# Performance work log

Hardware: AMD Instinct MI355X
Metric: run time of the kernel (lower is better)

## Reference

```python
import jax, jax.numpy as jnp
from jax import lax
import numpy as np

B, N, D = 8, 8192, 64
NPOINT, RADIUS, NSAMPLE = 1024, 0.2, 32
EPS = 1e-5  # BatchNorm eps


def setup_inputs() -> dict:
    key = jax.random.key(0)
    ks = jax.random.split(key, 8)
    inp = {
        "xyz": jax.random.uniform(ks[0], (B, 3, N), dtype=jnp.float32),
        "points": jax.random.normal(ks[1], (B, D, N), dtype=jnp.float32),
    }
    dims = [(3 + D, 64), (64, 64), (64, 128)]
    for i, (ci, co) in enumerate(dims):
        inp[f"w{i}"] = jax.random.normal(ks[2 + i], (co, ci), dtype=jnp.float32) * float(1.0 / np.sqrt(ci))
        inp[f"b{i}"] = jnp.zeros((co,), jnp.float32)
        inp[f"g{i}"] = jnp.ones((co,), jnp.float32)
        inp[f"beta{i}"] = jnp.zeros((co,), jnp.float32)
    return inp


def _fps(xyz):
    # Farthest point sampling. xyz: [B, N, 3] -> idx [B, NPOINT]
    b = xyz.shape[0]

    def step(carry, _):
        dist, farthest = carry  # dist [B,N], farthest [B]
        centroid = jnp.take_along_axis(xyz, farthest[:, None, None], axis=1)  # [B,1,3]
        d = jnp.sum((xyz - centroid) ** 2, axis=-1)  # [B,N]
        dist = jnp.minimum(dist, d)
        return (dist, jnp.argmax(dist, axis=-1).astype(jnp.int32)), farthest

    init = (jnp.full((b, xyz.shape[1]), 1e10, xyz.dtype), jnp.zeros((b,), jnp.int32))
    _, idxs = lax.scan(step, init, None, length=NPOINT)  # [NPOINT, B]
    return idxs.T  # [B, NPOINT]


def _ball_query(new_xyz, xyz):
    # new_xyz: [B,S,3] centers, xyz: [B,N,3] -> neighbor idx [B,S,NSAMPLE]
    n = xyz.shape[1]
    sqr = jnp.sum((new_xyz[:, :, None, :] - xyz[:, None, :, :]) ** 2, axis=-1)  # [B,S,N]
    cand = jnp.where(sqr > RADIUS * RADIUS, n, jnp.arange(n, dtype=jnp.int32))  # N = invalid
    neg_top, _ = lax.top_k(-cand, NSAMPLE)  # smallest NSAMPLE valid indices
    idx = -neg_top  # [B,S,K], ascending; == n where fewer than K neighbors
    first = idx[..., :1]  # pad with first (closest-by-index) valid neighbor
    return jnp.where(idx == n, first, idx)


def reference(xyz, points, w0, b0, g0, beta0, w1, b1, g1, beta1, w2, b2, g2, beta2):
    xyz_t = jnp.transpose(xyz, (0, 2, 1))      # [B,N,3]
    pts_t = jnp.transpose(points, (0, 2, 1))   # [B,N,D]
    fps_idx = _fps(xyz_t)                      # [B,S]
    bidx = jnp.arange(xyz.shape[0])[:, None]
    new_xyz = xyz_t[bidx, fps_idx]             # [B,S,3]
    idx = _ball_query(new_xyz, xyz_t)          # [B,S,K]
    bidx3 = jnp.arange(xyz.shape[0])[:, None, None]
    grouped_xyz = xyz_t[bidx3, idx]            # [B,S,K,3]
    grouped_norm = grouped_xyz - new_xyz[:, :, None, :]
    grouped_pts = pts_t[bidx3, idx]            # [B,S,K,D]
    feat = jnp.concatenate([grouped_norm, grouped_pts], axis=-1)  # [B,S,K,3+D]
    # shared 1x1 Conv + BatchNorm (training-mode batch stats) + ReLU chain
    for w, b, g, bt in ((w0, b0, g0, beta0), (w1, b1, g1, beta1), (w2, b2, g2, beta2)):
        h = jnp.einsum('bskc,oc->bsko', feat, w) + b
        mean = jnp.mean(h, axis=(0, 1, 2), keepdims=True)
        var = jnp.var(h, axis=(0, 1, 2), keepdims=True)
        feat = jax.nn.relu((h - mean) * lax.rsqrt(var + EPS) * g + bt)
    pooled = jnp.max(feat, axis=2)             # max over NSAMPLE -> [B,S,C_out]
    return jnp.transpose(new_xyz, (0, 2, 1)), jnp.transpose(pooled, (0, 2, 1))
```

## Files before the change

kernel.cpp:

```cpp
#include <hip/hip_runtime.h>

#define NB 8
#define NP 8192
#define SP 1024
#define KS 32
#define CD 64
#define MROWS (NB*SP*KS)
#define NCOPY 16

typedef float v2f __attribute__((ext_vector_type(2)));
typedef unsigned long long u64;

template <int CTRL>
__device__ __forceinline__ u64 dpp_max_step(u64 x) {
    int lo = (int)(unsigned)(x & 0xffffffffull);
    int hi = (int)(unsigned)(x >> 32);
    int slo = __builtin_amdgcn_update_dpp(lo, lo, CTRL, 0xf, 0xf, false);
    int shi = __builtin_amdgcn_update_dpp(hi, hi, CTRL, 0xf, 0xf, false);
    u64 y = ((u64)(unsigned)shi << 32) | (unsigned)slo;
    return x > y ? x : y;
}

__global__ __launch_bounds__(512, 1) void k_fps_pre(const float* __restrict__ xyz,
                                                    float* __restrict__ fps_pts,
                                                    float* __restrict__ out_nx,
                                                    const float* __restrict__ points,
                                                    float* __restrict__ pts_t,
                                                    const float* __restrict__ w0,
                                                    const float* __restrict__ w1,
                                                    const float* __restrict__ w2,
                                                    float* __restrict__ Wt0,
                                                    float* __restrict__ Wt1,
                                                    float* __restrict__ Wt2,
                                                    float* __restrict__ stats)
{
#pragma clang fp contract(off)
    __shared__ __align__(16) unsigned char smem[131072 + 256];
    const int blk = blockIdx.x;
    const int t = threadIdx.x;

    if (blk >= NB) {
        if (blk >= NB + NB * (NP / 64)) {
            for (int i = t; i < 8192; i += 512) stats[i] = 0.f;
            for (int i = t; i < 64 * 67; i += 512) { int c = i / 67, kk = i % 67; Wt0[kk * 64 + c] = w0[i]; }
            for (int i = t; i < 64 * 64; i += 512) { int c = i >> 6, kk = i & 63; Wt1[kk * 64 + c] = w1[i]; }
            for (int i = t; i < 128 * 64; i += 512) { int c = i >> 6, kk = i & 63; Wt2[kk * 128 + c] = w2[i]; }
            return;
        }
        float (*tile)[65] = (float(*)[65])smem;
        const int tblk = blk - NB;
        const int b = tblk >> 7;
        const int n0 = (tblk & 127) << 6;
        const float* pb = points + (size_t)b * CD * NP;
        const int c = t & 63;
        const int dr = t >> 6;
#pragma unroll
        for (int it = 0; it < 8; ++it) {
            int d = dr + it * 8;
            tile[d][c] = pb[(size_t)d * NP + n0 + c];
        }
        __syncthreads();
#pragma unroll
        for (int it = 0; it < 8; ++it) {
            int nn = dr + it * 8;
            pts_t[((size_t)b * NP + n0 + nn) * CD + c] = tile[c][nn];
        }
        return;
    }

    float4* s_p = (float4*)smem;
    u64 (*s_wk)[8] = (u64(*)[8])(smem + 131072);
    const int b = blk;
    const int lane = t & 63, wid = t >> 6;
    const float* xb = xyz + (size_t)b * 3 * NP;
    v2f px[8], py[8], pz[8], dv[8];
#pragma unroll
    for (int j = 0; j < 8; ++j) {
        const int n0 = t + (2 * j) * 512, n1 = n0 + 512;
        px[j] = (v2f){xb[n0], xb[n1]};
        py[j] = (v2f){xb[NP + n0], xb[NP + n1]};
        pz[j] = (v2f){xb[2 * NP + n0], xb[2 * NP + n1]};
        dv[j] = (v2f){1e10f, 1e10f};
        s_p[n0] = make_float4(px[j].x, py[j].x, pz[j].x, 0.f);
        s_p[n1] = make_float4(px[j].y, py[j].y, pz[j].y, 0.f);
    }
    float cx = xb[0], cy = xb[NP], cz = xb[2 * NP];
    float hx0 = 0.f, hy0 = 0.f, hz0 = 0.f;
    float hx1 = 0.f, hy1 = 0.f, hz1 = 0.f;
    __syncthreads();
    for (int i = 0; i < SP; ++i) {
        if (i == t)       { hx0 = cx; hy0 = cy; hz0 = cz; }
        if (i == t + 512) { hx1 = cx; hy1 = cy; hz1 = cz; }
        float bv = -1.f; int bg = 0;
#pragma unroll
        for (int j = 0; j < 8; ++j) {
            v2f dx = px[j] - cx;
            v2f dy = py[j] - cy;
            v2f dz = pz[j] - cz;
            v2f d  = dx * dx + dy * dy;
            d = d + dz * dz;
            v2f dm = dv[j];
            dm.x = fminf(dm.x, d.x);
            dm.y = fminf(dm.y, d.y);
            dv[j] = dm;
            if (dm.x > bv) { bv = dm.x; bg = t + (2 * j) * 512; }
            if (dm.y > bv) { bv = dm.y; bg = t + (2 * j + 1) * 512; }
        }
        u64 bk = ((u64)__float_as_uint(bv) << 32) | (unsigned int)~bg;
        bk = dpp_max_step<0x111>(bk);
        bk = dpp_max_step<0x112>(bk);
        bk = dpp_max_step<0x114>(bk);
        bk = dpp_max_step<0x118>(bk);
        bk = dpp_max_step<0x142>(bk);
        bk = dpp_max_step<0x143>(bk);
        const int par = i & 1;
        if (lane == 63) s_wk[par][wid] = bk;
        __syncthreads();
        u64 rk = s_wk[par][lane & 7];
        rk = dpp_max_step<0x111>(rk);
        rk = dpp_max_step<0x112>(rk);
        rk = dpp_max_step<0x114>(rk);
        rk = dpp_max_step<0x118>(rk);
        const int wg = ~__builtin_amdgcn_readlane((int)(unsigned)(rk & 0xffffffffull), 15);
        const float4 c = s_p[wg];
        cx = c.x; cy = c.y; cz = c.z;
    }
    fps_pts[(b * SP + t) * 3 + 0] = hx0;
    fps_pts[(b * SP + t) * 3 + 1] = hy0;
    fps_pts[(b * SP + t) * 3 + 2] = hz0;
    fps_pts[(b * SP + t + 512) * 3 + 0] = hx1;
    fps_pts[(b * SP + t + 512) * 3 + 1] = hy1;
    fps_pts[(b * SP + t + 512) * 3 + 2] = hz1;
    out_nx[(size_t)b * 3 * SP + 0 * SP + t] = hx0;
    out_nx[(size_t)b * 3 * SP + 1 * SP + t] = hy0;
    out_nx[(size_t)b * 3 * SP + 2 * SP + t] = hz0;
    out_nx[(size_t)b * 3 * SP + 0 * SP + t + 512] = hx1;
    out_nx[(size_t)b * 3 * SP + 1 * SP + t + 512] = hy1;
    out_nx[(size_t)b * 3 * SP + 2 * SP + t + 512] = hz1;
}

__global__ __launch_bounds__(256) void k_ballquery(const float* __restrict__ xyz,
                                                   const float* __restrict__ fps_pts,
                                                   int* __restrict__ ball_idx)
{
    const int wib = threadIdx.x >> 6;
    const int lane = threadIdx.x & 63;
    const int wid = blockIdx.x * 4 + wib;
    const int b = wid >> 10;
    const float* xb = xyz + (size_t)b * 3 * NP;
    const float qx = fps_pts[wid * 3 + 0];
    const float qy = fps_pts[wid * 3 + 1];
    const float qz = fps_pts[wid * 3 + 2];
    __shared__ int s_list[4][KS];
    int* list = s_list[wib];
    const float r2 = (float)(0.2 * 0.2);
    int found = 0;
    for (int base = 0; base < NP && found < KS; base += 64) {
        int n = base + lane;
        float dx = __fsub_rn(qx, xb[n]);
        float dy = __fsub_rn(qy, xb[NP + n]);
        float dz = __fsub_rn(qz, xb[2 * NP + n]);
        float d = __fadd_rn(__fadd_rn(__fmul_rn(dx, dx), __fmul_rn(dy, dy)), __fmul_rn(dz, dz));
        bool in = !(d > r2);
        unsigned long long m = __ballot(in);
        int before = __popcll(m & ((1ull << lane) - 1ull));
        int pos = found + before;
        if (in && pos < KS) list[pos] = n;
        found += __popcll(m);
    }
    int first = list[0];
    if (lane < KS) {
        int v = (lane < found) ? list[lane] : first;
        ball_idx[wid * KS + lane] = v;
    }
}

__global__ __launch_bounds__(256) void k_layer1(const float* __restrict__ xyz,
                                                const float* __restrict__ pts_t,
                                                const float* __restrict__ fps_pts,
                                                const int* __restrict__ ball_idx,
                                                const float* __restrict__ Wt0,
                                                const float* __restrict__ bias0,
                                                float* __restrict__ h1,
                                                float* __restrict__ sum0,
                                                float* __restrict__ ssq0)
{
    __shared__ __align__(16) float Ft[67 * 128];
    __shared__ __align__(16) float Ws[67 * 64];
    __shared__ int   s_idx[128];
    __shared__ float s_q[4][3];
    const int t = threadIdx.x;
    const int m0 = blockIdx.x * 128;
    const int g0 = m0 >> 5;
    const int b = g0 >> 10;
    if (t < 128) s_idx[t] = ball_idx[g0 * KS + t];
    if (t < 12) ((float*)s_q)[t] = fps_pts[g0 * 3 + t];
    for (int i = t; i < 67 * 64; i += 256) Ws[i] = Wt0[i];
    __syncthreads();
    {
        const int r = t >> 1, half = t & 1;
        const int n = s_idx[r];
        const float* prow = pts_t + ((size_t)b * NP + n) * CD;
#pragma unroll
        for (int rep = 0; rep < 8; ++rep) {
            const int c4 = half * 4 + rep * 8;
            float4 v = *(const float4*)(prow + c4);
            Ft[(3 + c4 + 0) * 128 + r] = v.x;
            Ft[(3 + c4 + 1) * 128 + r] = v.y;
            Ft[(3 + c4 + 2) * 128 + r] = v.z;
            Ft[(3 + c4 + 3) * 128 + r] = v.w;
        }
        if (t < 128) {
            const int n2 = s_idx[t];
            const int g = t >> 5;
            const float* xb = xyz + (size_t)b * 3 * NP;
            Ft[0 * 128 + t] = __fsub_rn(xb[n2],          s_q[g][0]);
            Ft[1 * 128 + t] = __fsub_rn(xb[NP + n2],     s_q[g][1]);
            Ft[2 * 128 + t] = __fsub_rn(xb[2 * NP + n2], s_q[g][2]);
        }
    }
    __syncthreads();
    const int rg = t >> 3;
    const int cg = t & 7;
    float4 ba = *(const float4*)(bias0 + cg * 8);
    float4 bb = *(const float4*)(bias0 + cg * 8 + 4);
    float acc[4][8];
#pragma unroll
    for (int j = 0; j < 4; ++j) {
        acc[j][0] = ba.x; acc[j][1] = ba.y; acc[j][2] = ba.z; acc[j][3] = ba.w;
        acc[j][4] = bb.x; acc[j][5] = bb.y; acc[j][6] = bb.z; acc[j][7] = bb.w;
    }
    for (int kk = 0; kk < 67; ++kk) {
        float4 f = *(const float4*)(Ft + kk * 128 + rg * 4);
        float4 wa = *(const float4*)(Ws + kk * 64 + cg * 8);
        float4 wb = *(const float4*)(Ws + kk * 64 + cg * 8 + 4);
        float fv[4] = {f.x, f.y, f.z, f.w};
        float wv[8] = {wa.x, wa.y, wa.z, wa.w, wb.x, wb.y, wb.z, wb.w};
#pragma unroll
        for (int j = 0; j < 4; ++j)
#pragma unroll
            for (int i = 0; i < 8; ++i) acc[j][i] = fmaf(fv[j], wv[i], acc[j][i]);
    }
    float ls[8] = {0,0,0,0,0,0,0,0}, lq[8] = {0,0,0,0,0,0,0,0};
#pragma unroll
    for (int j = 0; j < 4; ++j) {
        int m = m0 + rg * 4 + j;
        float4 oa = {acc[j][0], acc[j][1], acc[j][2], acc[j][3]};
        float4 ob = {acc[j][4], acc[j][5], acc[j][6], acc[j][7]};
        *(float4*)(h1 + (size_t)m * 64 + cg * 8) = oa;
        *(float4*)(h1 + (size_t)m * 64 + cg * 8 + 4) = ob;
#pragma unroll
        for (int i = 0; i < 8; ++i) { float v = acc[j][i]; ls[i] += v; lq[i] += v * v; }
    }
    __syncthreads();
    float* part_s = Ft;
    float* part_q = Ft + 2048;
#pragma unroll
    for (int i = 0; i < 8; ++i) { part_s[rg * 64 + cg * 8 + i] = ls[i]; part_q[rg * 64 + cg * 8 + i] = lq[i]; }
    __syncthreads();
    if (t < 64) {
        float s = 0.f, q = 0.f;
#pragma unroll
        for (int rgi = 0; rgi < 32; ++rgi) { s += part_s[rgi * 64 + t]; q += part_q[rgi * 64 + t]; }
        int cp = blockIdx.x & (NCOPY - 1);
        atomicAdd(&sum0[cp * 64 + t], s);
        atomicAdd(&ssq0[cp * 64 + t], q);
    }
}

__global__ __launch_bounds__(256) void k_layer2(const float* __restrict__ h1,
                                                const float* __restrict__ Wt1,
                                                const float* __restrict__ bias1,
                                                const float* __restrict__ ss1,
                                                float* __restrict__ h2,
                                                float* __restrict__ sum1,
                                                float* __restrict__ ssq1)
{
    __shared__ __align__(16) float Ft[64 * 128];
    __shared__ __align__(16) float Ws[64 * 64];
    __shared__ float s_sc[64], s_sh[64];
    const int t = threadIdx.x;
    const int m0 = blockIdx.x * 128;
    for (int i = t; i < 64 * 64; i += 256) Ws[i] = Wt1[i];
    if (t < 64) { s_sc[t] = ss1[t]; s_sh[t] = ss1[64 + t]; }
    __syncthreads();
    {
        const int tq = t >> 2, qq = t & 3;
#pragma unroll
        for (int rr = 0; rr < 2; ++rr) {
            const int r = rr * 64 + tq;
            const float* hrow = h1 + (size_t)(m0 + r) * 64;
#pragma unroll
            for (int rep = 0; rep < 4; ++rep) {
                const int c4 = qq * 4 + rep * 16;
                float4 v = *(const float4*)(hrow + c4);
                Ft[(c4 + 0) * 128 + r] = fmaxf(0.f, fmaf(v.x, s_sc[c4 + 0], s_sh[c4 + 0]));
                Ft[(c4 + 1) * 128 + r] = fmaxf(0.f, fmaf(v.y, s_sc[c4 + 1], s_sh[c4 + 1]));
                Ft[(c4 + 2) * 128 + r] = fmaxf(0.f, fmaf(v.z, s_sc[c4 + 2], s_sh[c4 + 2]));
                Ft[(c4 + 3) * 128 + r] = fmaxf(0.f, fmaf(v.w, s_sc[c4 + 3], s_sh[c4 + 3]));
// ... 184 lines not shown
    float rstd = 1.0f / sqrtf(var + 1e-5f);
    float scale = g[c] * rstd;
    ss[c] = scale;
    ss[nc + c] = beta[c] - mean * scale;
}

extern "C" void kernel_launch(void* const* d_in, const int* in_sizes, int n_in,
                              void* d_out, int out_size, void* d_ws, size_t ws_size,
                              hipStream_t stream)
{
    const float* xyz    = (const float*)d_in[0];
    const float* points = (const float*)d_in[1];
    const float* w0 = (const float*)d_in[2];
    const float* b0 = (const float*)d_in[3];
    const float* gm0 = (const float*)d_in[4];
    const float* bt0 = (const float*)d_in[5];
    const float* w1 = (const float*)d_in[6];
    const float* b1 = (const float*)d_in[7];
    const float* gm1 = (const float*)d_in[8];
    const float* bt1 = (const float*)d_in[9];
    const float* w2 = (const float*)d_in[10];
    const float* b2 = (const float*)d_in[11];
    const float* gm2 = (const float*)d_in[12];
    const float* bt2 = (const float*)d_in[13];
    float* out = (float*)d_out;

    char* p = (char*)d_ws;
    auto alloc = [&](size_t nbytes) -> void* {
        void* r = (void*)p;
        p += (nbytes + 255) & ~(size_t)255;
        return r;
    };
    float* fps_pts = (float*)alloc((size_t)NB * SP * 3 * 4);
    int*   ball_idx = (int*)alloc((size_t)NB * SP * KS * 4);
    float* pts_t = (float*)alloc((size_t)NB * NP * CD * 4);
    float* h1 = (float*)alloc((size_t)MROWS * 64 * 4);
    float* h2 = (float*)alloc((size_t)MROWS * 64 * 4);
    float* gmax = (float*)alloc((size_t)NB * SP * 128 * 4);
    float* gmin = (float*)alloc((size_t)NB * SP * 128 * 4);
    float* Wt0 = (float*)alloc(67 * 64 * 4);
    float* Wt1 = (float*)alloc(64 * 64 * 4);
    float* Wt2 = (float*)alloc(64 * 128 * 4);
    float* stats = (float*)alloc(8192 * 4);
    float* ss1 = (float*)alloc(128 * 4);
    float* ss2 = (float*)alloc(128 * 4);
    float* ss3 = (float*)alloc(256 * 4);

    float* sum0 = stats;
    float* ssq0 = stats + 16 * 64;
    float* sum1 = stats + 2 * 16 * 64;
    float* ssq1 = stats + 3 * 16 * 64;
    float* sum2 = stats + 4 * 16 * 64;
    float* ssq2 = sum2 + 16 * 128;

    k_fps_pre<<<NB + NB * (NP / 64) + 1, 512, 0, stream>>>(
        xyz, fps_pts, out, points, pts_t, w0, w1, w2, Wt0, Wt1, Wt2, stats);
    k_ballquery<<<(NB * SP) / 4, 256, 0, stream>>>(xyz, fps_pts, ball_idx);
    k_layer1<<<MROWS / 128, 256, 0, stream>>>(xyz, pts_t, fps_pts, ball_idx, Wt0, b0, h1, sum0, ssq0);
    k_finalize<<<1, 128, 0, stream>>>(sum0, ssq0, gm0, bt0, ss1, 64);
    k_layer2<<<MROWS / 128, 256, 0, stream>>>(h1, Wt1, b1, ss1, h2, sum1, ssq1);
    k_finalize<<<1, 128, 0, stream>>>(sum1, ssq1, gm1, bt1, ss2, 64);
    k_layer3<<<MROWS / 128, 256, 0, stream>>>(h2, Wt2, b2, ss2, sum2, ssq2, gmax, gmin);
    k_finalize<<<1, 128, 0, stream>>>(sum2, ssq2, gm2, bt2, ss3, 128);
    k_pool2<<<(NB * SP * 128) / 256, 256, 0, stream>>>(gmax, gmin, ss3, out + 24576);
}
```

Before: 1.217 ms.

## Split FPS argmax into float max then index min, use packed-math distance asm

The FPS loop now reduces a plain float max across the wavefront with DPP, then finds the matching slot and reduces the smallest global index in a separate 32-bit DPP pass. This replaces the 64-bit key shuffles and the per-element index tracking. Distances are computed with inline packed-f32 asm using negated centroids. The cross-wave reduction is shortened by one step, and selected centroids are written out by thread 0 on each iteration instead of being buffered per thread. The intent is to shorten the serial per-iteration critical path of FPS, at the cost of extra compare and select work and per-iteration global stores.

```diff
diff --git a/kernel.cpp b/kernel.cpp
--- a/kernel.cpp
+++ b/kernel.cpp
@@ -19,6 +19,19 @@
     int shi = __builtin_amdgcn_update_dpp(hi, hi, CTRL, 0xf, 0xf, false);
     u64 y = ((u64)(unsigned)shi << 32) | (unsigned)slo;
     return x > y ? x : y;
+}
+
+template <int CTRL>
+__device__ __forceinline__ float dpp_fmax_step(float x) {
+    int xi = __float_as_int(x);
+    int s = __builtin_amdgcn_update_dpp(xi, xi, CTRL, 0xf, 0xf, false);
+    return fmaxf(x, __int_as_float(s));
+}
+
+template <int CTRL>
+__device__ __forceinline__ int dpp_imin_step(int x) {
+    int s = __builtin_amdgcn_update_dpp(x, x, CTRL, 0xf, 0xf, false);
+    return s < x ? s : x;
 }
 
 __global__ __launch_bounds__(512, 1) void k_fps_pre(const float* __restrict__ xyz,
@@ -73,6 +86,8 @@
     const int b = blk;
     const int lane = t & 63, wid = t >> 6;
     const float* xb = xyz + (size_t)b * 3 * NP;
+    float* fp_b = fps_pts + (size_t)b * SP * 3;
+    float* nx_b = out_nx + (size_t)b * 3 * SP;
     v2f px[8], py[8], pz[8], dv[8];
 #pragma unroll
     for (int j = 0; j < 8; ++j) {
@@ -84,59 +99,81 @@
         s_p[n0] = make_float4(px[j].x, py[j].x, pz[j].x, 0.f);
         s_p[n1] = make_float4(px[j].y, py[j].y, pz[j].y, 0.f);
     }
-    float cx = xb[0], cy = xb[NP], cz = xb[2 * NP];
-    float hx0 = 0.f, hy0 = 0.f, hz0 = 0.f;
-    float hx1 = 0.f, hy1 = 0.f, hz1 = 0.f;
+    {
+        const float cx = xb[0], cy = xb[NP], cz = xb[2 * NP];
+        if (t == 0) {
+            fp_b[0] = cx; fp_b[1] = cy; fp_b[2] = cz;
+            nx_b[0] = cx; nx_b[SP] = cy; nx_b[2 * SP] = cz;
+        }
+    }
+    v2f ncx = (v2f){-xb[0], -xb[0]};
+    v2f ncy = (v2f){-xb[NP], -xb[NP]};
+    v2f ncz = (v2f){-xb[2 * NP], -xb[2 * NP]};
     __syncthreads();
     for (int i = 0; i < SP; ++i) {
-        if (i == t)       { hx0 = cx; hy0 = cy; hz0 = cz; }
-        if (i == t + 512) { hx1 = cx; hy1 = cy; hz1 = cz; }
-        float bv = -1.f; int bg = 0;
+        float bv = -1.f;
 #pragma unroll
         for (int j = 0; j < 8; ++j) {
-            v2f dx = px[j] - cx;
-            v2f dy = py[j] - cy;
-            v2f dz = pz[j] - cz;
-            v2f d  = dx * dx + dy * dy;
-            d = d + dz * dz;
+            v2f t0, t1, d;
+            asm("v_pk_add_f32 %0, %3, %6\n\t"
+                "v_pk_add_f32 %1, %4, %7\n\t"
+                "v_pk_add_f32 %2, %5, %8\n\t"
+                "v_pk_mul_f32 %0, %0, %0\n\t"
+                "v_pk_mul_f32 %1, %1, %1\n\t"
+                "v_pk_add_f32 %0, %0, %1\n\t"
+                "v_pk_mul_f32 %2, %2, %2\n\t"
+                "v_pk_add_f32 %2, %2, %0"
+                : "=&v"(t0), "=&v"(t1), "=&v"(d)
+                : "v"(px[j]), "v"(py[j]), "v"(pz[j]), "v"(ncx), "v"(ncy), "v"(ncz));
             v2f dm = dv[j];
             dm.x = fminf(dm.x, d.x);
             dm.y = fminf(dm.y, d.y);
             dv[j] = dm;
-            if (dm.x > bv) { bv = dm.x; bg = t + (2 * j) * 512; }
-            if (dm.y > bv) { bv = dm.y; bg = t + (2 * j + 1) * 512; }
-        }
-        u64 bk = ((u64)__float_as_uint(bv) << 32) | (unsigned int)~bg;
-        bk = dpp_max_step<0x111>(bk);
-        bk = dpp_max_step<0x112>(bk);
-        bk = dpp_max_step<0x114>(bk);
-        bk = dpp_max_step<0x118>(bk);
-        bk = dpp_max_step<0x142>(bk);
-        bk = dpp_max_step<0x143>(bk);
+            bv = fmaxf(bv, fmaxf(dm.x, dm.y));
+        }
+        float wv = bv;
+        wv = dpp_fmax_step<0x111>(wv);
+        wv = dpp_fmax_step<0x112>(wv);
+        wv = dpp_fmax_step<0x114>(wv);
+        wv = dpp_fmax_step<0x118>(wv);
+        wv = dpp_fmax_step<0x142>(wv);
+        wv = dpp_fmax_step<0x143>(wv);
+        const float Wv = __int_as_float(__builtin_amdgcn_readlane(__float_as_int(wv), 63));
+        int slot = 16;
+#pragma unroll
+        for (int j = 7; j >= 0; --j) {
+            if (dv[j].y == Wv) slot = 2 * j + 1;
+            if (dv[j].x == Wv) slot = 2 * j;
+        }
+        int gid = (slot << 9) | t;
+        gid = dpp_imin_step<0x111>(gid);
+        gid = dpp_imin_step<0x112>(gid);
+        gid = dpp_imin_step<0x114>(gid);
+        gid = dpp_imin_step<0x118>(gid);
+        gid = dpp_imin_step<0x142>(gid);
+        gid = dpp_imin_step<0x143>(gid);
         const int par = i & 1;
-        if (lane == 63) s_wk[par][wid] = bk;
+        if (lane == 63)
+            s_wk[par][wid] = ((u64)(unsigned)__float_as_int(wv) << 32) | (unsigned)~gid;
         __syncthreads();
         u64 rk = s_wk[par][lane & 7];
         rk = dpp_max_step<0x111>(rk);
         rk = dpp_max_step<0x112>(rk);
         rk = dpp_max_step<0x114>(rk);
-        rk = dpp_max_step<0x118>(rk);
-        const int wg = ~__builtin_amdgcn_readlane((int)(unsigned)(rk & 0xffffffffull), 15);
+        const int wg = ~__builtin_amdgcn_readlane((int)(unsigned)(rk & 0xffffffffull), 7);
         const float4 c = s_p[wg];
-        cx = c.x; cy = c.y; cz = c.z;
-    }
-    fps_pts[(b * SP + t) * 3 + 0] = hx0;
-    fps_pts[(b * SP + t) * 3 + 1] = hy0;
-    fps_pts[(b * SP + t) * 3 + 2] = hz0;
-    fps_pts[(b * SP + t + 512) * 3 + 0] = hx1;
-    fps_pts[(b * SP + t + 512) * 3 + 1] = hy1;
-    fps_pts[(b * SP + t + 512) * 3 + 2] = hz1;
-    out_nx[(size_t)b * 3 * SP + 0 * SP + t] = hx0;
-    out_nx[(size_t)b * 3 * SP + 1 * SP + t] = hy0;
-    out_nx[(size_t)b * 3 * SP + 2 * SP + t] = hz0;
-    out_nx[(size_t)b * 3 * SP + 0 * SP + t + 512] = hx1;
-    out_nx[(size_t)b * 3 * SP + 1 * SP + t + 512] = hy1;
-    out_nx[(size_t)b * 3 * SP + 2 * SP + t + 512] = hz1;
+        if (t == 0 && i + 1 < SP) {
+            fp_b[(i + 1) * 3 + 0] = c.x;
+            fp_b[(i + 1) * 3 + 1] = c.y;
+            fp_b[(i + 1) * 3 + 2] = c.z;
+            nx_b[i + 1] = c.x;
+            nx_b[SP + i + 1] = c.y;
+            nx_b[2 * SP + i + 1] = c.z;
+        }
+        ncx = (v2f){-c.x, -c.x};
+        ncy = (v2f){-c.y, -c.y};
+        ncz = (v2f){-c.z, -c.z};
+    }
 }
 
 __global__ __launch_bounds__(256) void k_ballquery(const float* __restrict__ xyz,
```

New measurement: 1.327 ms. +9.0%, slower.

## Fuse FPS, ball query and layer1 into persistent producer-consumer megakernel

Applied to the files above, without the earlier changes.

Merges farthest point sampling, ball query and the first conv layer into one persistent kernel. Eight blocks run FPS and publish sampled centroids in chunks of 32 through global atomics and a progress counter. The remaining blocks take work items from an atomic ticket, spin until their centroids are ready, then run the ball query and layer1 GEMM, so this work overlaps with the serial FPS. In exchange it adds spin-waiting, atomic traffic and reduced occupancy (512-thread blocks, half idle in the GEMM). It also depends on all 256 blocks being co-resident, or it can deadlock.

```diff
diff --git a/kernel.cpp b/kernel.cpp
--- a/kernel.cpp
+++ b/kernel.cpp
@@ -21,250 +21,280 @@
     return x > y ? x : y;
 }
 
-__global__ __launch_bounds__(512, 1) void k_fps_pre(const float* __restrict__ xyz,
-                                                    float* __restrict__ fps_pts,
-                                                    float* __restrict__ out_nx,
-                                                    const float* __restrict__ points,
-                                                    float* __restrict__ pts_t,
-                                                    const float* __restrict__ w0,
-                                                    const float* __restrict__ w1,
-                                                    const float* __restrict__ w2,
-                                                    float* __restrict__ Wt0,
-                                                    float* __restrict__ Wt1,
-                                                    float* __restrict__ Wt2,
-                                                    float* __restrict__ stats)
-{
-#pragma clang fp contract(off)
-    __shared__ __align__(16) unsigned char smem[131072 + 256];
+__global__ __launch_bounds__(512) void k_pre(const float* __restrict__ points,
+                                             float* __restrict__ pts_t,
+                                             const float* __restrict__ w0,
+                                             const float* __restrict__ w1,
+                                             const float* __restrict__ w2,
+                                             float* __restrict__ Wt0,
+                                             float* __restrict__ Wt1,
+                                             float* __restrict__ Wt2,
+                                             float* __restrict__ stats,
+                                             int* __restrict__ ctl)
+{
+    __shared__ float tile[64][65];
     const int blk = blockIdx.x;
     const int t = threadIdx.x;
-
-    if (blk >= NB) {
-        if (blk >= NB + NB * (NP / 64)) {
-            for (int i = t; i < 8192; i += 512) stats[i] = 0.f;
-            for (int i = t; i < 64 * 67; i += 512) { int c = i / 67, kk = i % 67; Wt0[kk * 64 + c] = w0[i]; }
-            for (int i = t; i < 64 * 64; i += 512) { int c = i >> 6, kk = i & 63; Wt1[kk * 64 + c] = w1[i]; }
-            for (int i = t; i < 128 * 64; i += 512) { int c = i >> 6, kk = i & 63; Wt2[kk * 128 + c] = w2[i]; }
-            return;
-        }
-        float (*tile)[65] = (float(*)[65])smem;
-        const int tblk = blk - NB;
-        const int b = tblk >> 7;
-        const int n0 = (tblk & 127) << 6;
-        const float* pb = points + (size_t)b * CD * NP;
-        const int c = t & 63;
-        const int dr = t >> 6;
-#pragma unroll
-        for (int it = 0; it < 8; ++it) {
-            int d = dr + it * 8;
-            tile[d][c] = pb[(size_t)d * NP + n0 + c];
-        }
-        __syncthreads();
-#pragma unroll
-        for (int it = 0; it < 8; ++it) {
-            int nn = dr + it * 8;
-            pts_t[((size_t)b * NP + n0 + nn) * CD + c] = tile[c][nn];
-        }
+    if (blk >= NB * (NP / 64)) {
+        for (int i = t; i < 8192; i += 512) stats[i] = 0.f;
+        if (t < 64) ctl[t] = 0;
+        for (int i = t; i < 64 * 67; i += 512) { int c = i / 67, kk = i % 67; Wt0[kk * 64 + c] = w0[i]; }
+        for (int i = t; i < 64 * 64; i += 512) { int c = i >> 6, kk = i & 63; Wt1[kk * 64 + c] = w1[i]; }
+        for (int i = t; i < 128 * 64; i += 512) { int c = i >> 6, kk = i & 63; Wt2[kk * 128 + c] = w2[i]; }
         return;
     }
-
-    float4* s_p = (float4*)smem;
-    u64 (*s_wk)[8] = (u64(*)[8])(smem + 131072);
-    const int b = blk;
+    const int b = blk >> 7;
+    const int n0 = (blk & 127) << 6;
+    const float* pb = points + (size_t)b * CD * NP;
+    const int c = t & 63;
+    const int dr = t >> 6;
+#pragma unroll
+    for (int it = 0; it < 8; ++it) {
+        int d = dr + it * 8;
+        tile[d][c] = pb[(size_t)d * NP + n0 + c];
+    }
+    __syncthreads();
+#pragma unroll
+    for (int it = 0; it < 8; ++it) {
+        int nn = dr + it * 8;
+        pts_t[((size_t)b * NP + n0 + nn) * CD + c] = tile[c][nn];
+    }
+}
+
+__global__ __launch_bounds__(512, 1) void k_mega(const float* __restrict__ xyz,
+                                                 float* __restrict__ fps_pts,
+                                                 float* __restrict__ out_nx,
+                                                 const float* __restrict__ pts_t,
+                                                 const float* __restrict__ Wt0,
+                                                 const float* __restrict__ bias0,
+                                                 float* __restrict__ h1,
+                                                 float* __restrict__ sum0,
+                                                 float* __restrict__ ssq0,
+                                                 int* __restrict__ ctl)
+{
+#pragma clang fp contract(off)
+    __shared__ __align__(16) unsigned char smem[131344];
+    const int blk = blockIdx.x;
+    const int t = threadIdx.x;
     const int lane = t & 63, wid = t >> 6;
-    const float* xb = xyz + (size_t)b * 3 * NP;
-    v2f px[8], py[8], pz[8], dv[8];
-#pragma unroll
-    for (int j = 0; j < 8; ++j) {
-        const int n0 = t + (2 * j) * 512, n1 = n0 + 512;
-        px[j] = (v2f){xb[n0], xb[n1]};
-        py[j] = (v2f){xb[NP + n0], xb[NP + n1]};
-        pz[j] = (v2f){xb[2 * NP + n0], xb[2 * NP + n1]};
-        dv[j] = (v2f){1e10f, 1e10f};
-        s_p[n0] = make_float4(px[j].x, py[j].x, pz[j].x, 0.f);
-        s_p[n1] = make_float4(px[j].y, py[j].y, pz[j].y, 0.f);
-    }
-    float cx = xb[0], cy = xb[NP], cz = xb[2 * NP];
-    float hx0 = 0.f, hy0 = 0.f, hz0 = 0.f;
-    float hx1 = 0.f, hy1 = 0.f, hz1 = 0.f;
-    __syncthreads();
-    for (int i = 0; i < SP; ++i) {
-        if (i == t)       { hx0 = cx; hy0 = cy; hz0 = cz; }
-        if (i == t + 512) { hx1 = cx; hy1 = cy; hz1 = cz; }
-        float bv = -1.f; int bg = 0;
+    unsigned int* fpu = (unsigned int*)fps_pts;
+
+    if (blk < NB) {
+        float4* s_p = (float4*)smem;
+        u64 (*s_wk)[8] = (u64(*)[8])(smem + 131072);
+        const int b = blk;
+        const float* xb = xyz + (size_t)b * 3 * NP;
+        v2f px[8], py[8], pz[8], dv[8];
 #pragma unroll
         for (int j = 0; j < 8; ++j) {
-            v2f dx = px[j] - cx;
-            v2f dy = py[j] - cy;
-            v2f dz = pz[j] - cz;
-            v2f d  = dx * dx + dy * dy;
-            d = d + dz * dz;
-            v2f dm = dv[j];
-            dm.x = fminf(dm.x, d.x);
-            dm.y = fminf(dm.y, d.y);
-            dv[j] = dm;
-            if (dm.x > bv) { bv = dm.x; bg = t + (2 * j) * 512; }
-            if (dm.y > bv) { bv = dm.y; bg = t + (2 * j + 1) * 512; }
-        }
-        u64 bk = ((u64)__float_as_uint(bv) << 32) | (unsigned int)~bg;
-        bk = dpp_max_step<0x111>(bk);
-        bk = dpp_max_step<0x112>(bk);
-        bk = dpp_max_step<0x114>(bk);
-        bk = dpp_max_step<0x118>(bk);
-        bk = dpp_max_step<0x142>(bk);
-        bk = dpp_max_step<0x143>(bk);
-        const int par = i & 1;
-        if (lane == 63) s_wk[par][wid] = bk;
-        __syncthreads();
-        u64 rk = s_wk[par][lane & 7];
-        rk = dpp_max_step<0x111>(rk);
-        rk = dpp_max_step<0x112>(rk);
-        rk = dpp_max_step<0x114>(rk);
-        rk = dpp_max_step<0x118>(rk);
-        const int wg = ~__builtin_amdgcn_readlane((int)(unsigned)(rk & 0xffffffffull), 15);
-        const float4 c = s_p[wg];
-        cx = c.x; cy = c.y; cz = c.z;
-    }
-    fps_pts[(b * SP + t) * 3 + 0] = hx0;
-    fps_pts[(b * SP + t) * 3 + 1] = hy0;
-    fps_pts[(b * SP + t) * 3 + 2] = hz0;
-    fps_pts[(b * SP + t + 512) * 3 + 0] = hx1;
-    fps_pts[(b * SP + t + 512) * 3 + 1] = hy1;
-    fps_pts[(b * SP + t + 512) * 3 + 2] = hz1;
-    out_nx[(size_t)b * 3 * SP + 0 * SP + t] = hx0;
-    out_nx[(size_t)b * 3 * SP + 1 * SP + t] = hy0;
-    out_nx[(size_t)b * 3 * SP + 2 * SP + t] = hz0;
-    out_nx[(size_t)b * 3 * SP + 0 * SP + t + 512] = hx1;
-    out_nx[(size_t)b * 3 * SP + 1 * SP + t + 512] = hy1;
-    out_nx[(size_t)b * 3 * SP + 2 * SP + t + 512] = hz1;
-}
-
-__global__ __launch_bounds__(256) void k_ballquery(const float* __restrict__ xyz,
-                                                   const float* __restrict__ fps_pts,
-                                                   int* __restrict__ ball_idx)
-{
-    const int wib = threadIdx.x >> 6;
-    const int lane = threadIdx.x & 63;
-    const int wid = blockIdx.x * 4 + wib;
-    const int b = wid >> 10;
-    const float* xb = xyz + (size_t)b * 3 * NP;
-    const float qx = fps_pts[wid * 3 + 0];
-    const float qy = fps_pts[wid * 3 + 1];
-    const float qz = fps_pts[wid * 3 + 2];
-    __shared__ int s_list[4][KS];
-    int* list = s_list[wib];
-    const float r2 = (float)(0.2 * 0.2);
-    int found = 0;
-    for (int base = 0; base < NP && found < KS; base += 64) {
-        int n = base + lane;
-        float dx = __fsub_rn(qx, xb[n]);
-        float dy = __fsub_rn(qy, xb[NP + n]);
-        float dz = __fsub_rn(qz, xb[2 * NP + n]);
-        float d = __fadd_rn(__fadd_rn(__fmul_rn(dx, dx), __fmul_rn(dy, dy)), __fmul_rn(dz, dz));
-        bool in = !(d > r2);
-        unsigned long long m = __ballot(in);
-        int before = __popcll(m & ((1ull << lane) - 1ull));
-        int pos = found + before;
-        if (in && pos < KS) list[pos] = n;
-        found += __popcll(m);
-    }
-    int first = list[0];
-    if (lane < KS) {
-        int v = (lane < found) ? list[lane] : first;
-        ball_idx[wid * KS + lane] = v;
-    }
-}
-
-__global__ __launch_bounds__(256) void k_layer1(const float* __restrict__ xyz,
-                                                const float* __restrict__ pts_t,
-                                                const float* __restrict__ fps_pts,
-                                                const int* __restrict__ ball_idx,
-                                                const float* __restrict__ Wt0,
-                                                const float* __restrict__ bias0,
-                                                float* __restrict__ h1,
-                                                float* __restrict__ sum0,
-                                                float* __restrict__ ssq0)
-{
-    __shared__ __align__(16) float Ft[67 * 128];
-    __shared__ __align__(16) float Ws[67 * 64];
-    __shared__ int   s_idx[128];
-    __shared__ float s_q[4][3];
-    const int t = threadIdx.x;
-    const int m0 = blockIdx.x * 128;
-    const int g0 = m0 >> 5;
-    const int b = g0 >> 10;
-    if (t < 128) s_idx[t] = ball_idx[g0 * KS + t];
-    if (t < 12) ((float*)s_q)[t] = fps_pts[g0 * 3 + t];
-    for (int i = t; i < 67 * 64; i += 256) Ws[i] = Wt0[i];
-    __syncthreads();
-    {
-        const int r = t >> 1, half = t & 1;
-        const int n = s_idx[r];
-        const float* prow = pts_t + ((size_t)b * NP + n) * CD;
-#pragma unroll
-        for (int rep = 0; rep < 8; ++rep) {
-            const int c4 = half * 4 + rep * 8;
-            float4 v = *(const float4*)(prow + c4);
-            Ft[(3 + c4 + 0) * 128 + r] = v.x;
-            Ft[(3 + c4 + 1) * 128 + r] = v.y;
-            Ft[(3 + c4 + 2) * 128 + r] = v.z;
-            Ft[(3 + c4 + 3) * 128 + r] = v.w;
-        }
-        if (t < 128) {
-            const int n2 = s_idx[t];
-            const int g = t >> 5;
-            const float* xb = xyz + (size_t)b * 3 * NP;
-            Ft[0 * 128 + t] = __fsub_rn(xb[n2],          s_q[g][0]);
-            Ft[1 * 128 + t] = __fsub_rn(xb[NP + n2],     s_q[g][1]);
-            Ft[2 * 128 + t] = __fsub_rn(xb[2 * NP + n2], s_q[g][2]);
-        }
-    }
-    __syncthreads();
-    const int rg = t >> 3;
-    const int cg = t & 7;
-    float4 ba = *(const float4*)(bias0 + cg * 8);
-    float4 bb = *(const float4*)(bias0 + cg * 8 + 4);
-    float acc[4][8];
-#pragma unroll
-    for (int j = 0; j < 4; ++j) {
-        acc[j][0] = ba.x; acc[j][1] = ba.y; acc[j][2] = ba.z; acc[j][3] = ba.w;
-        acc[j][4] = bb.x; acc[j][5] = bb.y; acc[j][6] = bb.z; acc[j][7] = bb.w;
-    }
-    for (int kk = 0; kk < 67; ++kk) {
-        float4 f = *(const float4*)(Ft + kk * 128 + rg * 4);
-        float4 wa = *(const float4*)(Ws + kk * 64 + cg * 8);
-        float4 wb = *(const float4*)(Ws + kk * 64 + cg * 8 + 4);
-        float fv[4] = {f.x, f.y, f.z, f.w};
-        float wv[8] = {wa.x, wa.y, wa.z, wa.w, wb.x, wb.y, wb.z, wb.w};
-#pragma unroll
-        for (int j = 0; j < 4; ++j)
-#pragma unroll
-            for (int i = 0; i < 8; ++i) acc[j][i] = fmaf(fv[j], wv[i], acc[j][i]);
-    }
-    float ls[8] = {0,0,0,0,0,0,0,0}, lq[8] = {0,0,0,0,0,0,0,0};
-#pragma unroll
-    for (int j = 0; j < 4; ++j) {
-        int m = m0 + rg * 4 + j;
-        float4 oa = {acc[j][0], acc[j][1], acc[j][2], acc[j][3]};
-        float4 ob = {acc[j][4], acc[j][5], acc[j][6], acc[j][7]};
-        *(float4*)(h1 + (size_t)m * 64 + cg * 8) = oa;
-        *(float4*)(h1 + (size_t)m * 64 + cg * 8 + 4) = ob;
-#pragma unroll
-        for (int i = 0; i < 8; ++i) { float v = acc[j][i]; ls[i] += v; lq[i] += v * v; }
-    }
-    __syncthreads();
-    float* part_s = Ft;
-    float* part_q = Ft + 2048;
-#pragma unroll
-    for (int i = 0; i < 8; ++i) { part_s[rg * 64 + cg * 8 + i] = ls[i]; part_q[rg * 64 + cg * 8 + i] = lq[i]; }
-    __syncthreads();
-    if (t < 64) {
-        float s = 0.f, q = 0.f;
-#pragma unroll
-        for (int rgi = 0; rgi < 32; ++rgi) { s += part_s[rgi * 64 + t]; q += part_q[rgi * 64 + t]; }
-        int cp = blockIdx.x & (NCOPY - 1);
-        atomicAdd(&sum0[cp * 64 + t], s);
-        atomicAdd(&ssq0[cp * 64 + t], q);
+            const int n0 = t + (2 * j) * 512, n1 = n0 + 512;
+            px[j] = (v2f){xb[n0], xb[n1]};
+            py[j] = (v2f){xb[NP + n0], xb[NP + n1]};
+            pz[j] = (v2f){xb[2 * NP + n0], xb[2 * NP + n1]};
+            dv[j] = (v2f){1e10f, 1e10f};
+            s_p[n0] = make_float4(px[j].x, py[j].x, pz[j].x, 0.f);
+            s_p[n1] = make_float4(px[j].y, py[j].y, pz[j].y, 0.f);
+        }
+        float cx = xb[0], cy = xb[NP], cz = xb[2 * NP];
+        float hx0 = 0.f, hy0 = 0.f, hz0 = 0.f;
+        float hx1 = 0.f, hy1 = 0.f, hz1 = 0.f;
+        __syncthreads();
+        for (int i = 0; i < SP; ++i) {
+            if (i == t)       { hx0 = cx; hy0 = cy; hz0 = cz; }
+            if (i == t + 512) { hx1 = cx; hy1 = cy; hz1 = cz; }
+            if ((i & 31) == 31) {
+                if (i < 512) {
+                    if (t >= i - 31 && t <= i) {
+                        unsigned int* dst = fpu + ((size_t)b * SP + t) * 3;
+                        atomicExch(dst + 0, __float_as_uint(hx0));
+                        atomicExch(dst + 1, __float_as_uint(hy0));
+                        atomicExch(dst + 2, __float_as_uint(hz0));
+                    }
+                } else {
+                    const int s = t + 512;
+                    if (s >= i - 31 && s <= i) {
+                        unsigned int* dst = fpu + ((size_t)b * SP + s) * 3;
+                        atomicExch(dst + 0, __float_as_uint(hx1));
+                        atomicExch(dst + 1, __float_as_uint(hy1));
+                        atomicExch(dst + 2, __float_as_uint(hz1));
+                    }
+                }
+            }
+            if ((i & 31) == 0 && i != 0 && t == 2) atomicExch(&ctl[8 + b], i);
+            float bv = -1.f; int bg = 0;
+#pragma unroll
+            for (int j = 0; j < 8; ++j) {
+                v2f dx = px[j] - cx;
+                v2f dy = py[j] - cy;
+                v2f dz = pz[j] - cz;
+                v2f d  = dx * dx + dy * dy;
+                d = d + dz * dz;
+                v2f dm = dv[j];
+                dm.x = fminf(dm.x, d.x);
+                dm.y = fminf(dm.y, d.y);
+                dv[j] = dm;
+                if (dm.x > bv) { bv = dm.x; bg = t + (2 * j) * 512; }
+                if (dm.y > bv) { bv = dm.y; bg = t + (2 * j + 1) * 512; }
+            }
+            u64 bk = ((u64)__float_as_uint(bv) << 32) | (unsigned int)~bg;
+            bk = dpp_max_step<0x111>(bk);
+            bk = dpp_max_step<0x112>(bk);
+            bk = dpp_max_step<0x114>(bk);
+            bk = dpp_max_step<0x118>(bk);
+            bk = dpp_max_step<0x142>(bk);
+            bk = dpp_max_step<0x143>(bk);
+            const int par = i & 1;
+            if (lane == 63) s_wk[par][wid] = bk;
+            __syncthreads();
+            u64 rk = s_wk[par][lane & 7];
+            rk = dpp_max_step<0x111>(rk);
+            rk = dpp_max_step<0x112>(rk);
+            rk = dpp_max_step<0x114>(rk);
+            rk = dpp_max_step<0x118>(rk);
+            const int wg = ~__builtin_amdgcn_readlane((int)(unsigned)(rk & 0xffffffffull), 15);
+            const float4 c = s_p[wg];
+            cx = c.x; cy = c.y; cz = c.z;
+        }
+        if (t == 2) atomicExch(&ctl[8 + b], SP);
+        out_nx[(size_t)b * 3 * SP + 0 * SP + t] = hx0;
+        out_nx[(size_t)b * 3 * SP + 1 * SP + t] = hy0;
+        out_nx[(size_t)b * 3 * SP + 2 * SP + t] = hz0;
+        out_nx[(size_t)b * 3 * SP + 0 * SP + t + 512] = hx1;
+        out_nx[(size_t)b * 3 * SP + 1 * SP + t + 512] = hy1;
+        out_nx[(size_t)b * 3 * SP + 2 * SP + t + 512] = hz1;
+        return;
+    }
+
+    float* Ft    = (float*)smem;
+    float* Ws    = (float*)(smem + 34304);
+    int*   s_idx = (int*)(smem + 51456);
+    float* s_q   = (float*)(smem + 51968);
+    int*   s_tk  = (int*)(smem + 131328);
+    int*   s_rdy = (int*)(smem + 131332);
+
+    for (int i = t; i < 67 * 64; i += 512) Ws[i] = Wt0[i];
+
+    for (;;) {
+        __syncthreads();
+        if (t == 0) *s_tk = atomicAdd(&ctl[1], 1);
+        __syncthreads();
+        const int u = *s_tk;
+        if (u >= 2048) break;
+        const int b = u & 7, kq = u >> 3;
+        const int need = 4 * kq + 4;
+        const int g0 = b * SP + kq * 4;
+        for (;;) {
+            if (t == 0) *s_rdy = (atomicAdd(&ctl[8 + b], 0) >= need);
+            __syncthreads();
+            const int ok = *s_rdy;
+            __syncthreads();
+            if (ok) break;
+            __builtin_amdgcn_s_sleep(32);
+        }
+        if (t < 12) {
+            unsigned int uv = atomicAdd(fpu + (size_t)g0 * 3 + t, 0u);
+            s_q[t] = __uint_as_float(uv);
+        }
+        __syncthreads();
+        if (wid < 4) {
+            const float qx = s_q[wid * 3 + 0];
+            const float qy = s_q[wid * 3 + 1];
+            const float qz = s_q[wid * 3 + 2];
+            const float* xbq = xyz + (size_t)b * 3 * NP;
+            int* list = s_idx + wid * KS;
+            const float r2 = (float)(0.2 * 0.2);
+            int found = 0;
+            for (int base2 = 0; base2 < NP && found < KS; base2 += 64) {
+                int n = base2 + lane;
+                float dx = __fsub_rn(qx, xbq[n]);
+                float dy = __fsub_rn(qy, xbq[NP + n]);
+                float dz = __fsub_rn(qz, xbq[2 * NP + n]);
+                float d = __fadd_rn(__fadd_rn(__fmul_rn(dx, dx), __fmul_rn(dy, dy)), __fmul_rn(dz, dz));
+                bool in = !(d > r2);
+                unsigned long long m = __ballot(in);
+                int before = __popcll(m & ((1ull << lane) - 1ull));
+                int pos = found + before;
+                if (in && pos < KS) list[pos] = n;
+                found += __popcll(m);
+            }
+            int first = list[0];
+            if (lane < KS) { int v = (lane < found) ? list[lane] : first; list[lane] = v; }
+        }
+        __syncthreads();
+        const size_t m0 = (size_t)g0 * KS;
+        if (t < 256) {
+            const int r = t >> 1, half = t & 1;
+            const int n = s_idx[r];
+            const float* prow = pts_t + ((size_t)b * NP + n) * CD;
+#pragma unroll
+            for (int rep = 0; rep < 8; ++rep) {
+                const int c4 = half * 4 + rep * 8;
+                float4 v = *(const float4*)(prow + c4);
+                Ft[(3 + c4 + 0) * 128 + r] = v.x;
+                Ft[(3 + c4 + 1) * 128 + r] = v.y;
+                Ft[(3 + c4 + 2) * 128 + r] = v.z;
+                Ft[(3 + c4 + 3) * 128 + r] = v.w;
+            }
+            if (t < 128) {
+                const int n2 = s_idx[t];
+                const int g = t >> 5;
+                const float* xbg = xyz + (size_t)b * 3 * NP;
+                Ft[0 * 128 + t] = __fsub_rn(xbg[n2],          s_q[g * 3 + 0]);
+                Ft[1 * 128 + t] = __fsub_rn(xbg[NP + n2],     s_q[g * 3 + 1]);
+                Ft[2 * 128 + t] = __fsub_rn(xbg[2 * NP + n2], s_q[g * 3 + 2]);
+            }
+        }
+        __syncthreads();
+        const int rg = t >> 3;
+        const int cg = t & 7;
+        float ls[8] = {0,0,0,0,0,0,0,0}, lq[8] = {0,0,0,0,0,0,0,0};
+        if (t < 256) {
+            float4 ba = *(const float4*)(bias0 + cg * 8);
+            float4 bb = *(const float4*)(bias0 + cg * 8 + 4);
+            float acc[4][8];
+#pragma unroll
+            for (int j = 0; j < 4; ++j) {
+                acc[j][0] = ba.x; acc[j][1] = ba.y; acc[j][2] = ba.z; acc[j][3] = ba.w;
+                acc[j][4] = bb.x; acc[j][5] = bb.y; acc[j][6] = bb.z; acc[j][7] = bb.w;
+            }
+            for (int kk = 0; kk < 67; ++kk) {
+                float4 f = *(const float4*)(Ft + kk * 128 + rg * 4);
+                float4 wa = *(const float4*)(Ws + kk * 64 + cg * 8);
+                float4 wb = *(const float4*)(Ws + kk * 64 + cg * 8 + 4);
+                float fv[4] = {f.x, f.y, f.z, f.w};
+                float wv[8] = {wa.x, wa.y, wa.z, wa.w, wb.x, wb.y, wb.z, wb.w};
+#pragma unroll
+                for (int j = 0; j < 4; ++j)
+#pragma unroll
+                    for (int i = 0; i < 8; ++i) acc[j][i] = fmaf(fv[j], wv[i], acc[j][i]);
+            }
+#pragma unroll
+            for (int j = 0; j < 4; ++j) {
+                size_t m = m0 + rg * 4 + j;
+                float4 oa = {acc[j][0], acc[j][1], acc[j][2], acc[j][3]};
+                float4 ob = {acc[j][4], acc[j][5], acc[j][6], acc[j][7]};
+                *(float4*)(h1 + m * 64 + cg * 8) = oa;
+                *(float4*)(h1 + m * 64 + cg * 8 + 4) = ob;
+#pragma unroll
+                for (int i = 0; i < 8; ++i) { float v = acc[j][i]; ls[i] += v; lq[i] += v * v; }
+            }
+        }
+        __syncthreads();
+        float* part_s = Ft;
+        float* part_q = Ft + 2048;
+        if (t < 256) {
+#pragma unroll
+            for (int i = 0; i < 8; ++i) { part_s[rg * 64 + cg * 8 + i] = ls[i]; part_q[rg * 64 + cg * 8 + i] = lq[i]; }
+        }
+        __syncthreads();
+        if (t < 64) {
+            float s = 0.f, q = 0.f;
+#pragma unroll
+            for (int rgi = 0; rgi < 32; ++rgi) { s += part_s[rgi * 64 + t]; q += part_q[rgi * 64 + t]; }
+            int cp = kq & (NCOPY - 1);
+            atomicAdd(&sum0[cp * 64 + t], s);
+            atomicAdd(&ssq0[cp * 64 + t], q);
+        }
     }
 }
 
@@ -515,7 +545,6 @@
         return r;
     };
     float* fps_pts = (float*)alloc((size_t)NB * SP * 3 * 4);
-    int*   ball_idx = (int*)alloc((size_t)NB * SP * KS * 4);
     float* pts_t = (float*)alloc((size_t)NB * NP * CD * 4);
     float* h1 = (float*)alloc((size_t)MROWS * 64 * 4);
     float* h2 = (float*)alloc((size_t)MROWS * 64 * 4);
@@ -528,6 +557,7 @@
     float* ss1 = (float*)alloc(128 * 4);
     float* ss2 = (float*)alloc(128 * 4);
     float* ss3 = (float*)alloc(256 * 4);
+    int*   ctl = (int*)alloc(256);
 
     float* sum0 = stats;
     float* ssq0 = stats + 16 * 64;
@@ -536,10 +566,8 @@
     float* sum2 = stats + 4 * 16 * 64;
     float* ssq2 = sum2 + 16 * 128;
 
-    k_fps_pre<<<NB + NB * (NP / 64) + 1, 512, 0, stream>>>(
-        xyz, fps_pts, out, points, pts_t, w0, w1, w2, Wt0, Wt1, Wt2, stats);
-    k_ballquery<<<(NB * SP) / 4, 256, 0, stream>>>(xyz, fps_pts, ball_idx);
-    k_layer1<<<MROWS / 128, 256, 0, stream>>>(xyz, pts_t, fps_pts, ball_idx, Wt0, b0, h1, sum0, ssq0);
+    k_pre<<<NB * (NP / 64) + 1, 512, 0, stream>>>(points, pts_t, w0, w1, w2, Wt0, Wt1, Wt2, stats, ctl);
+    k_mega<<<256, 512, 0, stream>>>(xyz, fps_pts, out, pts_t, Wt0, b0, h1, sum0, ssq0, ctl);
     k_finalize<<<1, 128, 0, stream>>>(sum0, ssq0, gm0, bt0, ss1, 64);
     k_layer2<<<MROWS / 128, 256, 0, stream>>>(h1, Wt1, b1, ss1, h2, sum1, ssq1);
     k_finalize<<<1, 128, 0, stream>>>(sum1, ssq1, gm1, bt1, ss2, 64);
```

After: 1.296 ms. 1.06x slower.

## Fuse ball query into layer-1 kernel with warp-specialized 512-thread blocks

Applied to the files above, without the earlier changes.

Removes the separate ball-query kernel and its global index buffer. Each layer-1 block now uses 512 threads: four waves run the ball query for the block's four centroids straight into shared memory, while the other four waves load the weight matrix. This drops one kernel launch and the write and re-read of the neighbor indices. In exchange, half of each block sits idle during the GEMM, and the larger block may reduce occupancy.

```diff
diff --git a/kernel.cpp b/kernel.cpp
--- a/kernel.cpp
+++ b/kernel.cpp
@@ -139,46 +139,9 @@
     out_nx[(size_t)b * 3 * SP + 2 * SP + t + 512] = hz1;
 }
 
-__global__ __launch_bounds__(256) void k_ballquery(const float* __restrict__ xyz,
-                                                   const float* __restrict__ fps_pts,
-                                                   int* __restrict__ ball_idx)
-{
-    const int wib = threadIdx.x >> 6;
-    const int lane = threadIdx.x & 63;
-    const int wid = blockIdx.x * 4 + wib;
-    const int b = wid >> 10;
-    const float* xb = xyz + (size_t)b * 3 * NP;
-    const float qx = fps_pts[wid * 3 + 0];
-    const float qy = fps_pts[wid * 3 + 1];
-    const float qz = fps_pts[wid * 3 + 2];
-    __shared__ int s_list[4][KS];
-    int* list = s_list[wib];
-    const float r2 = (float)(0.2 * 0.2);
-    int found = 0;
-    for (int base = 0; base < NP && found < KS; base += 64) {
-        int n = base + lane;
-        float dx = __fsub_rn(qx, xb[n]);
-        float dy = __fsub_rn(qy, xb[NP + n]);
-        float dz = __fsub_rn(qz, xb[2 * NP + n]);
-        float d = __fadd_rn(__fadd_rn(__fmul_rn(dx, dx), __fmul_rn(dy, dy)), __fmul_rn(dz, dz));
-        bool in = !(d > r2);
-        unsigned long long m = __ballot(in);
-        int before = __popcll(m & ((1ull << lane) - 1ull));
-        int pos = found + before;
-        if (in && pos < KS) list[pos] = n;
-        found += __popcll(m);
-    }
-    int first = list[0];
-    if (lane < KS) {
-        int v = (lane < found) ? list[lane] : first;
-        ball_idx[wid * KS + lane] = v;
-    }
-}
-
-__global__ __launch_bounds__(256) void k_layer1(const float* __restrict__ xyz,
+__global__ __launch_bounds__(512) void k_layer1(const float* __restrict__ xyz,
                                                 const float* __restrict__ pts_t,
                                                 const float* __restrict__ fps_pts,
-                                                const int* __restrict__ ball_idx,
                                                 const float* __restrict__ Wt0,
                                                 const float* __restrict__ bias0,
                                                 float* __restrict__ h1,
@@ -188,16 +151,42 @@
     __shared__ __align__(16) float Ft[67 * 128];
     __shared__ __align__(16) float Ws[67 * 64];
     __shared__ int   s_idx[128];
-    __shared__ float s_q[4][3];
+    __shared__ float s_q[12];
     const int t = threadIdx.x;
+    const int lane = t & 63, wid = t >> 6;
     const int m0 = blockIdx.x * 128;
     const int g0 = m0 >> 5;
     const int b = g0 >> 10;
-    if (t < 128) s_idx[t] = ball_idx[g0 * KS + t];
-    if (t < 12) ((float*)s_q)[t] = fps_pts[g0 * 3 + t];
-    for (int i = t; i < 67 * 64; i += 256) Ws[i] = Wt0[i];
-    __syncthreads();
-    {
+    if (t < 12) s_q[t] = fps_pts[g0 * 3 + t];
+    __syncthreads();
+    if (wid < 4) {
+        const float qx = s_q[wid * 3 + 0];
+        const float qy = s_q[wid * 3 + 1];
+        const float qz = s_q[wid * 3 + 2];
+        const float* xbq = xyz + (size_t)b * 3 * NP;
+        int* list = s_idx + wid * KS;
+        const float r2 = (float)(0.2 * 0.2);
+        int found = 0;
+        for (int base2 = 0; base2 < NP && found < KS; base2 += 64) {
+            int n = base2 + lane;
+            float dx = __fsub_rn(qx, xbq[n]);
+            float dy = __fsub_rn(qy, xbq[NP + n]);
+            float dz = __fsub_rn(qz, xbq[2 * NP + n]);
+            float d = __fadd_rn(__fadd_rn(__fmul_rn(dx, dx), __fmul_rn(dy, dy)), __fmul_rn(dz, dz));
+            bool in = !(d > r2);
+            unsigned long long m = __ballot(in);
+            int before = __popcll(m & ((1ull << lane) - 1ull));
+            int pos = found + before;
+            if (in && pos < KS) list[pos] = n;
+            found += __popcll(m);
+        }
+        int first = list[0];
+        if (lane < KS) { int v = (lane < found) ? list[lane] : first; list[lane] = v; }
+    } else {
+        for (int i = t - 256; i < 67 * 64; i += 256) Ws[i] = Wt0[i];
+    }
+    __syncthreads();
+    if (t < 256) {
         const int r = t >> 1, half = t & 1;
         const int n = s_idx[r];
         const float* prow = pts_t + ((size_t)b * NP + n) * CD;
@@ -213,50 +202,54 @@
         if (t < 128) {
             const int n2 = s_idx[t];
             const int g = t >> 5;
-            const float* xb = xyz + (size_t)b * 3 * NP;
-            Ft[0 * 128 + t] = __fsub_rn(xb[n2],          s_q[g][0]);
-            Ft[1 * 128 + t] = __fsub_rn(xb[NP + n2],     s_q[g][1]);
-            Ft[2 * 128 + t] = __fsub_rn(xb[2 * NP + n2], s_q[g][2]);
+            const float* xbg = xyz + (size_t)b * 3 * NP;
+            Ft[0 * 128 + t] = __fsub_rn(xbg[n2],          s_q[g * 3 + 0]);
+            Ft[1 * 128 + t] = __fsub_rn(xbg[NP + n2],     s_q[g * 3 + 1]);
+            Ft[2 * 128 + t] = __fsub_rn(xbg[2 * NP + n2], s_q[g * 3 + 2]);
         }
     }
     __syncthreads();
     const int rg = t >> 3;
     const int cg = t & 7;
-    float4 ba = *(const float4*)(bias0 + cg * 8);
-    float4 bb = *(const float4*)(bias0 + cg * 8 + 4);
-    float acc[4][8];
-#pragma unroll
-    for (int j = 0; j < 4; ++j) {
-        acc[j][0] = ba.x; acc[j][1] = ba.y; acc[j][2] = ba.z; acc[j][3] = ba.w;
-        acc[j][4] = bb.x; acc[j][5] = bb.y; acc[j][6] = bb.z; acc[j][7] = bb.w;
-    }
-    for (int kk = 0; kk < 67; ++kk) {
-        float4 f = *(const float4*)(Ft + kk * 128 + rg * 4);
-        float4 wa = *(const float4*)(Ws + kk * 64 + cg * 8);
-        float4 wb = *(const float4*)(Ws + kk * 64 + cg * 8 + 4);
-        float fv[4] = {f.x, f.y, f.z, f.w};
-        float wv[8] = {wa.x, wa.y, wa.z, wa.w, wb.x, wb.y, wb.z, wb.w};
-#pragma unroll
-        for (int j = 0; j < 4; ++j)
-#pragma unroll
-            for (int i = 0; i < 8; ++i) acc[j][i] = fmaf(fv[j], wv[i], acc[j][i]);
-    }
     float ls[8] = {0,0,0,0,0,0,0,0}, lq[8] = {0,0,0,0,0,0,0,0};
-#pragma unroll
-    for (int j = 0; j < 4; ++j) {
-        int m = m0 + rg * 4 + j;
-        float4 oa = {acc[j][0], acc[j][1], acc[j][2], acc[j][3]};
-        float4 ob = {acc[j][4], acc[j][5], acc[j][6], acc[j][7]};
-        *(float4*)(h1 + (size_t)m * 64 + cg * 8) = oa;
-        *(float4*)(h1 + (size_t)m * 64 + cg * 8 + 4) = ob;
-#pragma unroll
-        for (int i = 0; i < 8; ++i) { float v = acc[j][i]; ls[i] += v; lq[i] += v * v; }
+    if (t < 256) {
+        float4 ba = *(const float4*)(bias0 + cg * 8);
+        float4 bb = *(const float4*)(bias0 + cg * 8 + 4);
+        float acc[4][8];
+#pragma unroll
+        for (int j = 0; j < 4; ++j) {
+            acc[j][0] = ba.x; acc[j][1] = ba.y; acc[j][2] = ba.z; acc[j][3] = ba.w;
+            acc[j][4] = bb.x; acc[j][5] = bb.y; acc[j][6] = bb.z; acc[j][7] = bb.w;
+        }
+        for (int kk = 0; kk < 67; ++kk) {
+            float4 f = *(const float4*)(Ft + kk * 128 + rg * 4);
+            float4 wa = *(const float4*)(Ws + kk * 64 + cg * 8);
+            float4 wb = *(const float4*)(Ws + kk * 64 + cg * 8 + 4);
+            float fv[4] = {f.x, f.y, f.z, f.w};
+            float wv[8] = {wa.x, wa.y, wa.z, wa.w, wb.x, wb.y, wb.z, wb.w};
+#pragma unroll
+            for (int j = 0; j < 4; ++j)
+#pragma unroll
+                for (int i = 0; i < 8; ++i) acc[j][i] = fmaf(fv[j], wv[i], acc[j][i]);
+        }
+#pragma unroll
+        for (int j = 0; j < 4; ++j) {
+            int m = m0 + rg * 4 + j;
+            float4 oa = {acc[j][0], acc[j][1], acc[j][2], acc[j][3]};
+            float4 ob = {acc[j][4], acc[j][5], acc[j][6], acc[j][7]};
+            *(float4*)(h1 + (size_t)m * 64 + cg * 8) = oa;
+            *(float4*)(h1 + (size_t)m * 64 + cg * 8 + 4) = ob;
+#pragma unroll
+            for (int i = 0; i < 8; ++i) { float v = acc[j][i]; ls[i] += v; lq[i] += v * v; }
+        }
     }
     __syncthreads();
     float* part_s = Ft;
     float* part_q = Ft + 2048;
-#pragma unroll
-    for (int i = 0; i < 8; ++i) { part_s[rg * 64 + cg * 8 + i] = ls[i]; part_q[rg * 64 + cg * 8 + i] = lq[i]; }
+    if (t < 256) {
+#pragma unroll
+        for (int i = 0; i < 8; ++i) { part_s[rg * 64 + cg * 8 + i] = ls[i]; part_q[rg * 64 + cg * 8 + i] = lq[i]; }
+    }
     __syncthreads();
     if (t < 64) {
         float s = 0.f, q = 0.f;
@@ -515,7 +508,6 @@
         return r;
     };
     float* fps_pts = (float*)alloc((size_t)NB * SP * 3 * 4);
-    int*   ball_idx = (int*)alloc((size_t)NB * SP * KS * 4);
     float* pts_t = (float*)alloc((size_t)NB * NP * CD * 4);
     float* h1 = (float*)alloc((size_t)MROWS * 64 * 4);
     float* h2 = (float*)alloc((size_t)MROWS * 64 * 4);
@@ -538,8 +530,7 @@
 
     k_fps_pre<<<NB + NB * (NP / 64) + 1, 512, 0, stream>>>(
         xyz, fps_pts, out, points, pts_t, w0, w1, w2, Wt0, Wt1, Wt2, stats);
-    k_ballquery<<<(NB * SP) / 4, 256, 0, stream>>>(xyz, fps_pts, ball_idx);
-    k_layer1<<<MROWS / 128, 256, 0, stream>>>(xyz, pts_t, fps_pts, ball_idx, Wt0, b0, h1, sum0, ssq0);
+    k_layer1<<<MROWS / 128, 512, 0, stream>>>(xyz, pts_t, fps_pts, Wt0, b0, h1, sum0, ssq0);
     k_finalize<<<1, 128, 0, stream>>>(sum0, ssq0, gm0, bt0, ss1, 64);
     k_layer2<<<MROWS / 128, 256, 0, stream>>>(h1, Wt1, b1, ss1, h2, sum1, ssq1);
     k_finalize<<<1, 128, 0, stream>>>(sum1, ssq1, gm1, bt1, ss2, 64);
```

Measured after the change: 1.235 ms. Within noise of the previous version (+1.5%).
